# Kernel optimization log

Measured on AMD Instinct MI355X. Metric: run time of the kernel, lower is better.

## Reference

```python
import jax, jax.numpy as jnp
import numpy as np

S_DIM, A_DIM, H_DIM = 256, 18, 256
E, NS, B = 5, 10, 4096  # ensemble, MC samples, batch


def setup_inputs() -> dict:
    key = jax.random.key(0)
    ks = iter(jax.random.split(key, 40))
    def kaiming(k, shape):
        return jax.random.normal(k, shape, jnp.float32) * np.float32(np.sqrt(2.0 / shape[-1]))
    inp = {
        "state": jax.random.normal(next(ks), (B, S_DIM), jnp.float32),
        "num_samples": NS,
    }
    dims = [(H_DIM, S_DIM), (H_DIM, H_DIM), (A_DIM, H_DIM)]
    for i, (o, ii) in enumerate(dims):
        inp[f"w_mu{i}"] = kaiming(next(ks), (E, o, ii))
        inp[f"w_rho{i}"] = jnp.full((E, o, ii), -3.0, jnp.float32)
        inp[f"b_mu{i}"] = jnp.zeros((E, o), jnp.float32)
        inp[f"b_rho{i}"] = jnp.full((E, o), -3.0, jnp.float32)
        inp[f"w_eps{i}"] = jax.random.normal(next(ks), (E, NS, o, ii), jnp.float32)
        inp[f"b_eps{i}"] = jax.random.normal(next(ks), (E, NS, o), jnp.float32)
    # uncertainty head: Linear(2A->H), ReLU, Linear(H->A), Softplus
    inp["uh_w1"] = kaiming(next(ks), (H_DIM, 2 * A_DIM))
    inp["uh_b1"] = jnp.zeros((H_DIM,), jnp.float32)
    inp["uh_w2"] = kaiming(next(ks), (A_DIM, H_DIM))
    inp["uh_b2"] = jnp.zeros((A_DIM,), jnp.float32)
    # risk head: Linear(3A->H), ReLU, Linear(H->1)
    inp["rh_w1"] = kaiming(next(ks), (H_DIM, 3 * A_DIM))
    inp["rh_b1"] = jnp.zeros((H_DIM,), jnp.float32)
    inp["rh_w2"] = kaiming(next(ks), (1, H_DIM))
    inp["rh_b2"] = jnp.zeros((1,), jnp.float32)
    return inp


def _kl(mu, sigma):
    # KL(N(mu, sigma) || N(0, 1)) summed over param dims -> per-ensemble [E]
    kl = -jnp.log(sigma) + (sigma ** 2 + mu ** 2) * 0.5 - 0.5
    return jnp.sum(kl, axis=tuple(range(1, mu.ndim)))


def _bayes(x, wmu, wrho, bmu, brho, weps, beps):
    # x: [E,S,B,in]; wmu: [E,out,in]; weps: [E,S,out,in]
    wsig = jax.nn.softplus(wrho)
    bsig = jax.nn.softplus(brho)
    w = wmu[:, None] + wsig[:, None] * weps        # [E,S,out,in]
    b = bmu[:, None] + bsig[:, None] * beps        # [E,S,out]
    y = jnp.einsum('esbi,esoi->esbo', x, w) + b[:, :, None, :]
    kl = _kl(wmu, wsig) + _kl(bmu, bsig)           # [E] (same for all MC samples)
    return y, kl


def reference(state, num_samples,
              w_mu0, w_rho0, b_mu0, b_rho0, w_eps0, b_eps0,
              w_mu1, w_rho1, b_mu1, b_rho1, w_eps1, b_eps1,
              w_mu2, w_rho2, b_mu2, b_rho2, w_eps2, b_eps2,
              uh_w1, uh_b1, uh_w2, uh_b2,
              rh_w1, rh_b1, rh_w2, rh_b2):
    e, ns = w_eps0.shape[0], w_eps0.shape[1]
    x = jnp.broadcast_to(state, (e, ns) + state.shape)          # [E,S,B,in]
    x, kl0 = _bayes(x, w_mu0, w_rho0, b_mu0, b_rho0, w_eps0, b_eps0)
    x = jax.nn.relu(x)  # dropout = identity (eval)
    x, kl1 = _bayes(x, w_mu1, w_rho1, b_mu1, b_rho1, w_eps1, b_eps1)
    x = jax.nn.relu(x)
    x, kl2 = _bayes(x, w_mu2, w_rho2, b_mu2, b_rho2, w_eps2, b_eps2)
    net_out = x.mean(axis=1)                                     # [E,B,A]
    q_mean = net_out.mean(axis=0)                                # [B,A]
    q_var = jnp.var(net_out, axis=0, ddof=1)                     # unbiased, as torch .var
    epistemic = q_var
    u_in = jnp.concatenate([q_mean, q_var], axis=-1)             # [B,2A]
    h = jax.nn.relu(u_in @ uh_w1.T + uh_b1)
    aleatoric = jax.nn.softplus(h @ uh_w2.T + uh_b2)             # [B,A]
    total_unc = epistemic + aleatoric
    r_in = jnp.concatenate([q_mean, epistemic, aleatoric], axis=-1)  # [B,3A]
    risk = jax.nn.relu(r_in @ rh_w1.T + rh_b1) @ rh_w2.T + rh_b2     # [B,1]
    s = 2.0 * jnp.sqrt(total_unc)
    lcb, ucb = q_mean - s, q_mean + s
    # total_kl = sum_e ns*kl_e ; divided by (E*num_samples) -> mean over ensemble
    kl_div = jnp.sum(kl0 + kl1 + kl2) / e
    return (q_mean, epistemic, aleatoric, total_unc, lcb, ucb, risk, kl_div)
```

## Files before the change

kernel.cpp:

```cpp
#include <hip/hip_runtime.h>
#include <hip/hip_bf16.h>


typedef __bf16 bf16x8 __attribute__((ext_vector_type(8)));
typedef float f32x4 __attribute__((ext_vector_type(4)));
typedef float f32x16 __attribute__((ext_vector_type(16)));
typedef unsigned short u16x4 __attribute__((ext_vector_type(4)));
typedef unsigned short u16x8 __attribute__((ext_vector_type(8)));

__device__ __forceinline__ unsigned short f2bf(float f) {
  unsigned int u = __builtin_bit_cast(unsigned int, f);
  u += 0x7fffu + ((u >> 16) & 1u);
  return (unsigned short)(u >> 16);
}

__device__ __forceinline__ float softplus_f(float x) {
  return (x > 20.f) ? x : __logf(1.f + __expf(x));
}

__device__ __forceinline__ float klterm(float m, float sg) {
  return -__logf(sg) + (sg * sg + m * m) * 0.5f - 0.5f;
}

__device__ __forceinline__ f32x16 mfma32(bf16x8 a, bf16x8 b, f32x16 c) {
  return __builtin_amdgcn_mfma_f32_32x32x16_bf16(a, b, c, 0, 0, 0);
}

template <int O>
__device__ __forceinline__ float wpanel_body(
    int p, int t, const float* __restrict__ wmu, const float* __restrict__ wrho,
    const float* __restrict__ weps, char* __restrict__ wf,
    char* __restrict__ lb) {
  int es = (O == 256) ? (p >> 3) : p;
  int osub = (O == 256) ? (p & 7) : 0;
  int e = es / 10, s = es - e * 10;
  float kl = 0.f;
  int i = (4 * t) & 255;
  int kt2 = i >> 4, byo = (i & 7) * 2, hi32 = 32 * ((i >> 3) & 1);
#pragma unroll
  for (int j = 0; j < 8; ++j) {
    int o = j * 4 + (t >> 6);
    int og = osub * 32 + o;
    float v[4];
    if (O == 256 || og < O) {
      size_t base = ((size_t)(e * O + og)) * 256 + i;
      f32x4 m4 = *(const f32x4*)(wmu + base);
      f32x4 r4 = *(const f32x4*)(wrho + base);
      f32x4 e4 = *(const f32x4*)(weps + ((size_t)((e * 10 + s) * O + og)) * 256 + i);
#pragma unroll
      for (int c = 0; c < 4; ++c) {
        float m = m4[c];
        float sg = softplus_f(r4[c]);
        v[c] = m + sg * e4[c];
        if (s == 0) kl += klterm(m, sg);
      }
    } else {
#pragma unroll
      for (int c = 0; c < 4; ++c) v[c] = 0.f;
    }
    u16x4 pk = {f2bf(v[0]), f2bf(v[1]), f2bf(v[2]), f2bf(v[3])};
    *(u16x4*)(lb + kt2 * 1024 + (o + hi32) * 16 + byo) = pk;
  }
  __syncthreads();
  char* dst = wf + (size_t)p * 16384;
#pragma unroll
  for (int j = 0; j < 4; ++j) {
    int idx = j * 256 + t;
    *(u16x8*)(dst + idx * 16) = *(const u16x8*)(lb + idx * 16);
  }
  return kl;
}

__device__ __forceinline__ void scvt_body(int gid, const float* __restrict__ s,
                                          unsigned short* __restrict__ d) {
  const f32x4* p = (const f32x4*)(s + (size_t)gid * 8);
  f32x4 x0 = p[0], x1 = p[1];
  u16x8 v = {f2bf(x0.x), f2bf(x0.y), f2bf(x0.z), f2bf(x0.w),
             f2bf(x1.x), f2bf(x1.y), f2bf(x1.z), f2bf(x1.w)};
  *(u16x8*)(d + (size_t)gid * 8) = v;
}

__global__ __launch_bounds__(256) void prep_kernel(
    const float* __restrict__ state, unsigned short* __restrict__ stateb,
    const float* __restrict__ wmu0, const float* __restrict__ wrho0,
    const float* __restrict__ weps0, char* __restrict__ W0f,
    const float* __restrict__ wmu1, const float* __restrict__ wrho1,
    const float* __restrict__ weps1, char* __restrict__ W1f,
    const float* __restrict__ wmu2, const float* __restrict__ wrho2,
    const float* __restrict__ weps2, char* __restrict__ W2f,
    const float* __restrict__ bmu0, const float* __restrict__ brho0,
    const float* __restrict__ beps0, const float* __restrict__ bmu1,
    const float* __restrict__ brho1, const float* __restrict__ beps1,
    const float* __restrict__ bmu2, const float* __restrict__ brho2,
    const float* __restrict__ beps2, float* __restrict__ bias0,
    float* __restrict__ bias1, float* __restrict__ bias2,
    float* __restrict__ partials) {
  __shared__ char lb[16384];
  int bid = blockIdx.x, t = threadIdx.x;
  float kl = 0.f;
  if (bid < 512) {
    scvt_body(bid * 256 + t, state, stateb);
  } else if (bid < 912) {
    kl = wpanel_body<256>(bid - 512, t, wmu0, wrho0, weps0, W0f, lb);
  } else if (bid < 1312) {
    kl = wpanel_body<256>(bid - 912, t, wmu1, wrho1, weps1, W1f, lb);
  } else if (bid < 1362) {
    kl = wpanel_body<18>(bid - 1312, t, wmu2, wrho2, weps2, W2f, lb);
  } else {
    int gid = (bid - 1362) * 256 + t;
    if (gid < 12800) {
      int es = gid >> 8, o = gid & 255, e = es / 10, s = es - e * 10;
      float m = bmu0[e * 256 + o];
      float sg = softplus_f(brho0[e * 256 + o]);
      bias0[gid] = m + sg * beps0[(e * 10 + s) * 256 + o];
      if (s == 0) kl = klterm(m, sg);
    } else if (gid < 25600) {
      int id = gid - 12800;
      int es = id >> 8, o = id & 255, e = es / 10, s = es - e * 10;
      float m = bmu1[e * 256 + o];
      float sg = softplus_f(brho1[e * 256 + o]);
      bias1[id] = m + sg * beps1[(e * 10 + s) * 256 + o];
      if (s == 0) kl = klterm(m, sg);
    } else if (gid < 27200) {
      int id = gid - 25600;
      int es = id >> 5, o = id & 31, e = es / 10, s = es - e * 10;
      if (o < 18) {
        float m = bmu2[e * 18 + o];
        float sg = softplus_f(brho2[e * 18 + o]);
        bias2[id] = m + sg * beps2[(e * 10 + s) * 18 + o];
        if (s == 0) kl = klterm(m, sg);
      } else {
        bias2[id] = 0.f;
      }
    }
  }
#pragma unroll
  for (int m = 32; m >= 1; m >>= 1) kl += __shfl_xor(kl, m);
  __shared__ float wsum[4];
  if ((t & 63) == 0) wsum[t >> 6] = kl;
  __syncthreads();
  if (t == 0) partials[bid] = wsum[0] + wsum[1] + wsum[2] + wsum[3];
}

__device__ __forceinline__ void mlp_layer1o(const char* __restrict__ wA,
                                            const float* __restrict__ bias_es,
                                            int w, char* __restrict__ buf,
                                            int lane) {
  const char* ap = wA + (size_t)w * 16384;
  int lo = lane * 16;
  f32x16 acc0, acc1, acc2, acc3;
#pragma unroll
  for (int c = 0; c < 16; ++c) {
    acc0[c] = 0.f; acc1[c] = 0.f; acc2[c] = 0.f; acc3[c] = 0.f;
  }

  bf16x8 ac = *(const bf16x8*)(ap + lo);
  bf16x8 b0c = *(const bf16x8*)(buf + lo);
  bf16x8 b1c = *(const bf16x8*)(buf + 16384 + lo);
  bf16x8 b2c = *(const bf16x8*)(buf + 32768 + lo);
  bf16x8 b3c = *(const bf16x8*)(buf + 49152 + lo);
#pragma unroll
  for (int kp = 0; kp < 8; ++kp) {
    bf16x8 an = *(const bf16x8*)(ap + (2 * kp + 1) * 1024 + lo);
    bf16x8 b0n = *(const bf16x8*)(buf + (2 * kp + 1) * 1024 + lo);
    bf16x8 b1n = *(const bf16x8*)(buf + 16384 + (2 * kp + 1) * 1024 + lo);
    bf16x8 b2n = *(const bf16x8*)(buf + 32768 + (2 * kp + 1) * 1024 + lo);
    bf16x8 b3n = *(const bf16x8*)(buf + 49152 + (2 * kp + 1) * 1024 + lo);
    __builtin_amdgcn_s_setprio(1);
    acc0 = mfma32(ac, b0c, acc0);
    acc1 = mfma32(ac, b1c, acc1);
    acc2 = mfma32(ac, b2c, acc2);
    acc3 = mfma32(ac, b3c, acc3);
    __builtin_amdgcn_s_setprio(0);
    if (kp < 7) {
      ac = *(const bf16x8*)(ap + (2 * kp + 2) * 1024 + lo);
      b0c = *(const bf16x8*)(buf + (2 * kp + 2) * 1024 + lo);
      b1c = *(const bf16x8*)(buf + 16384 + (2 * kp + 2) * 1024 + lo);
      b2c = *(const bf16x8*)(buf + 32768 + (2 * kp + 2) * 1024 + lo);
      b3c = *(const bf16x8*)(buf + 49152 + (2 * kp + 2) * 1024 + lo);
    }
    __builtin_amdgcn_s_setprio(1);
    acc0 = mfma32(an, b0n, acc0);
    acc1 = mfma32(an, b1n, acc1);
    acc2 = mfma32(an, b2n, acc2);
    acc3 = mfma32(an, b3n, acc3);
    __builtin_amdgcn_s_setprio(0);
  }
  __syncthreads();

  int hi = lane >> 5, bcol = lane & 31;
  int obt = w * 32;
  auto epi = [&](const f32x16& A, int bt) {
    char* fb = buf + (size_t)(bt * 16) * 1024;
#pragma unroll
    for (int q = 0; q < 4; ++q) {
      int o0 = obt + 8 * q + 4 * hi;
      f32x4 bv = *(const f32x4*)(bias_es + o0);
      float v0 = fmaxf(A[4 * q + 0] + bv.x, 0.f);
      float v1 = fmaxf(A[4 * q + 1] + bv.y, 0.f);
      float v2 = fmaxf(A[4 * q + 2] + bv.z, 0.f);
      float v3 = fmaxf(A[4 * q + 3] + bv.w, 0.f);
      u16x4 pk = {f2bf(v0), f2bf(v1), f2bf(v2), f2bf(v3)};
      int kt2t = o0 >> 4;
      *(u16x4*)(fb + kt2t * 1024 + (bcol + 32 * (q & 1)) * 16 + 8 * hi) = pk;
    }
  };
  epi(acc0, 0);
  epi(acc1, 1);
  epi(acc2, 2);
  epi(acc3, 3);
  __syncthreads();
}

__global__ __launch_bounds__(512, 4) void mlp_fused(
    const unsigned short* __restrict__ stateb, const char* __restrict__ W0f,
    const char* __restrict__ W1f, const char* __restrict__ W2f,
    const float* __restrict__ bias0, const float* __restrict__ bias1,
    const float* __restrict__ bias2, float* __restrict__ y2) {
  __shared__ char buf[65536];
  int tid = threadIdx.x, w = tid >> 6, lane = tid & 63;
  int lo = lane * 16;

  int bid = blockIdx.x;
  int lin = (bid & 7) * 200 + (bid >> 3);
  int es = lin >> 5, b0 = (lin & 31) * 128;

#pragma unroll
  for (int it = 0; it < 8; ++it) {
    int F = it * 8 + w, bt = F >> 4, kt2 = F & 15;
    const unsigned short* src =
        stateb + (size_t)(b0 + bt * 32 + (lane & 31)) * 256 + kt2 * 16 + (lane >> 5) * 8;
    *(u16x8*)(buf + F * 1024 + lo) = *(const u16x8*)src;
  }
  __syncthreads();

  mlp_layer1o(W0f + (size_t)es * 131072, bias0 + es * 256, w, buf, lane);
  mlp_layer1o(W1f + (size_t)es * 131072, bias1 + es * 256, w, buf, lane);

  if (w < 4) {
    int bt2 = w;
    f32x16 acc2;
#pragma unroll
    for (int c = 0; c < 16; ++c) acc2[c] = 0.f;
    const char* b2k = buf + (size_t)bt2 * 16384;
    const char* w2p = W2f + (size_t)es * 16384;
#pragma unroll
    for (int k = 0; k < 16; ++k) {
      bf16x8 a = *(const bf16x8*)(w2p + k * 1024 + lo);
      bf16x8 bb = *(const bf16x8*)(b2k + k * 1024 + lo);
      acc2 = mfma32(a, bb, acc2);
    }
    int hi = lane >> 5, bcol = lane & 31;
    int b_idx = b0 + bt2 * 32 + bcol;
    float* yp = y2 + ((size_t)es * 4096 + b_idx) * 20;
    float s[16];
#pragma unroll
    for (int q = 0; q < 4; ++q) {
      f32x4 bv = *(const f32x4*)(bias2 + es * 32 + 8 * q + 4 * hi);
      s[4 * q + 0] = acc2[4 * q + 0] + bv.x;
      s[4 * q + 1] = acc2[4 * q + 1] + bv.y;
      s[4 * q + 2] = acc2[4 * q + 2] + bv.z;
      s[4 * q + 3] = acc2[4 * q + 3] + bv.w;
    }
    if (hi == 0) {
      f32x4 v0 = {s[0], s[1], s[2], s[3]};
      f32x4 v1 = {s[4], s[5], s[6], s[7]};
      float2 v2 = {s[8], s[9]};
      *(f32x4*)(yp) = v0;
      *(f32x4*)(yp + 8) = v1;
      *(float2*)(yp + 16) = v2;
    } else {
      f32x4 v0 = {s[0], s[1], s[2], s[3]};
      f32x4 v1 = {s[4], s[5], s[6], s[7]};
      *(f32x4*)(yp + 4) = v0;
      *(f32x4*)(yp + 12) = v1;
    }
  }
}

__global__ __launch_bounds__(256) void heads_kernel(
    const float* __restrict__ y2, const float* __restrict__ partials,
    const float* __restrict__ uh_w1, const float* __restrict__ uh_b1,
    const float* __restrict__ uh_w2, const float* __restrict__ uh_b2,
    const float* __restrict__ rh_w1, const float* __restrict__ rh_b1,
    const float* __restrict__ rh_w2, const float* __restrict__ rh_b2,
    float* __restrict__ out) {
  int bid = blockIdx.x, t = threadIdx.x;
  if (bid == 512) {
    if (t < 64) {
      float acc = 0.f;
      for (int i = t; i < 1469; i += 64) acc += partials[i];
#pragma unroll
      for (int m = 32; m >= 1; m >>= 1) acc += __shfl_xor(acc, m);
      if (t == 0) out[446464] = acc * 0.2f;
    }
    return;
  }
  int b0 = bid * 8;

  __shared__ float ysh[8][1004];
  __shared__ float qsE[8][90];
  __shared__ float rin[8][56];
  __shared__ float h[8][260];

  for (int i = t; i < 2000; i += 256) {
    int r = i / 250, c = i - r * 250;
    int es_t = c / 5, part = c - es_t * 5;
    *(f32x4*)(&ysh[r][c * 4]) =
        *(const f32x4*)(y2 + ((size_t)es_t * 4096 + b0 + r) * 20 + part * 4);
  }
  __syncthreads();

  for (int i = t; i < 720; i += 256) {
    int r = i / 90, ae = i - r * 90;
    int a = ae / 5, e = ae - a * 5;
    float v = 0.f;
#pragma unroll
    for (int s = 0; s < 10; ++s) v += ysh[r][(e * 10 + s) * 20 + a];
    qsE[r][ae] = v * 0.1f;
  }
  __syncthreads();

  if (t < 144) {
    int r = t / 18, a = t - (t / 18) * 18;
    float qs = 0.f, qq = 0.f;
#pragma unroll
    for (int e = 0; e < 5; ++e) {
      float v = qsE[r][a * 5 + e];
      qs += v;
      qq += v * v;
    }
    float mean = qs * 0.2f;
    float var = fmaxf((qq - 5.f * mean * mean) * 0.25f, 0.f);
    rin[r][a] = mean;
    rin[r][18 + a] = var;
    out[(b0 + r) * 18 + a] = mean;
    out[73728 + (b0 + r) * 18 + a] = var;
  }
  __syncthreads();

  {
    f32x4 wv[9];
    const f32x4* wr = (const f32x4*)(uh_w1 + t * 36);
#pragma unroll
    for (int j = 0; j < 9; ++j) wv[j] = wr[j];
    float bb = uh_b1[t];
#pragma unroll
    for (int r = 0; r < 8; ++r) {
      float acc = bb;
#pragma unroll
      for (int j = 0; j < 9; ++j) {
        acc += wv[j].x * rin[r][j * 4] + wv[j].y * rin[r][j * 4 + 1] +
               wv[j].z * rin[r][j * 4 + 2] + wv[j].w * rin[r][j * 4 + 3];
      }
      h[r][t] = fmaxf(acc, 0.f);
    }
  }
  __syncthreads();

  if (t < 144) {
    int r = t / 18, a = t - (t / 18) * 18;
    float p = 0.f;
    const f32x4* w2r = (const f32x4*)(uh_w2 + a * 256);
#pragma unroll
    for (int j = 0; j < 64; ++j) {
      f32x4 wv = w2r[j];
      f32x4 hv = *(const f32x4*)(&h[r][j * 4]);
      p += wv.x * hv.x + wv.y * hv.y + wv.z * hv.z + wv.w * hv.w;
    }
    float alea = softplus_f(p + uh_b2[a]);
    float qm = rin[r][a], epi = rin[r][18 + a];
    float tu = epi + alea;
    float s2 = 2.f * sqrtf(tu);
    int b = b0 + r;
    out[2 * 73728 + b * 18 + a] = alea;
    out[3 * 73728 + b * 18 + a] = tu;
    out[4 * 73728 + b * 18 + a] = qm - s2;
    out[5 * 73728 + b * 18 + a] = qm + s2;
    rin[r][36 + a] = alea;
  }
  __syncthreads();

  {
    float w1v[54];
    const float2* wr2 = (const float2*)(rh_w1 + t * 54);
#pragma unroll
    for (int j = 0; j < 27; ++j) {
      float2 wv = wr2[j];
      w1v[j * 2] = wv.x;
      w1v[j * 2 + 1] = wv.y;
    }
    float bb = rh_b1[t];
#pragma unroll
    for (int r = 0; r < 8; ++r) {
      float acc = bb;
#pragma unroll
      for (int j = 0; j < 54; ++j) acc += w1v[j] * rin[r][j];
      h[r][t] = fmaxf(acc, 0.f);
    }
  }
  __syncthreads();

  if (t < 8) {
    float p = 0.f;
    const f32x4* w2r = (const f32x4*)(rh_w2);
#pragma unroll
    for (int j = 0; j < 64; ++j) {
      f32x4 wv = w2r[j];
      f32x4 hv = *(const f32x4*)(&h[t][j * 4]);
      p += wv.x * hv.x + wv.y * hv.y + wv.z * hv.z + wv.w * hv.w;
    }
    out[6 * 73728 + b0 + t] = p + rh_b2[0];
  }
}

extern "C" void kernel_launch(void* const* d_in, const int* in_sizes, int n_in,
                              void* d_out, int out_size, void* d_ws, size_t ws_size,
                              hipStream_t stream) {
  const float* state = (const float*)d_in[0];
  const float* w_mu0 = (const float*)d_in[2];
  const float* w_rho0 = (const float*)d_in[3];
  const float* b_mu0 = (const float*)d_in[4];
  const float* b_rho0 = (const float*)d_in[5];
  const float* w_eps0 = (const float*)d_in[6];
  const float* b_eps0 = (const float*)d_in[7];
  const float* w_mu1 = (const float*)d_in[8];
  const float* w_rho1 = (const float*)d_in[9];
  const float* b_mu1 = (const float*)d_in[10];
  const float* b_rho1 = (const float*)d_in[11];
  const float* w_eps1 = (const float*)d_in[12];
  const float* b_eps1 = (const float*)d_in[13];
  const float* w_mu2 = (const float*)d_in[14];
  const float* w_rho2 = (const float*)d_in[15];
  const float* b_mu2 = (const float*)d_in[16];
  const float* b_rho2 = (const float*)d_in[17];
  const float* w_eps2 = (const float*)d_in[18];
  const float* b_eps2 = (const float*)d_in[19];
  const float* uh_w1 = (const float*)d_in[20];
  const float* uh_b1 = (const float*)d_in[21];
  const float* uh_w2 = (const float*)d_in[22];
  const float* uh_b2 = (const float*)d_in[23];
  const float* rh_w1 = (const float*)d_in[24];
  const float* rh_b1 = (const float*)d_in[25];
  const float* rh_w2 = (const float*)d_in[26];
  const float* rh_b2 = (const float*)d_in[27];
  float* out = (float*)d_out;

  char* ws = (char*)d_ws;
  unsigned short* stateb = (unsigned short*)ws;
  char* W0f = ws + 2097152;
  char* W1f = W0f + 6553600;
  char* W2f = W1f + 6553600;
  float* bias0 = (float*)(W2f + 819200);
  float* bias1 = bias0 + 12800;
  float* bias2 = bias1 + 12800;
  float* y2 = bias2 + 1600;
  float* klpart = y2 + (size_t)50 * 4096 * 20;

  prep_kernel<<<1469, 256, 0, stream>>>(
      state, stateb, w_mu0, w_rho0, w_eps0, W0f, w_mu1, w_rho1, w_eps1, W1f,
      w_mu2, w_rho2, w_eps2, W2f, b_mu0, b_rho0, b_eps0, b_mu1, b_rho1, b_eps1,
      b_mu2, b_rho2, b_eps2, bias0, bias1, bias2, klpart);
  mlp_fused<<<1600, 512, 0, stream>>>(stateb, W0f, W1f, W2f, bias0, bias1,
                                      bias2, y2);
  heads_kernel<<<513, 256, 0, stream>>>(y2, klpart, uh_w1, uh_b1, uh_w2, uh_b2,
                                        rh_w1, rh_b1, rh_w2, rh_b2, out);
}
```

Measured before the change: 108.9 us.

## Stage weight tiles into LDS with async global_load_lds pipeline, halve batch tile

Packed layer-0/1 weights are reordered by k-slice so each 8 KB k-step across all output tiles is contiguous. The fused MLP kernel now streams these slices into a 4-deep LDS ring with global_load_lds, overlapping loads with MFMA instead of reading weights straight from global memory. The batch tile per block drops from 128 to 64 and the grid doubles to 3200 blocks, which halves the activation LDS footprint. The cost is a barrier per k-step, hand-written waitcnt bookkeeping, and twice as many weight reads from L2 across blocks.

```diff
diff --git a/kernel.cpp b/kernel.cpp
--- a/kernel.cpp
+++ b/kernel.cpp
@@ -24,6 +24,12 @@
 
 __device__ __forceinline__ f32x16 mfma32(bf16x8 a, bf16x8 b, f32x16 c) {
   return __builtin_amdgcn_mfma_f32_32x32x16_bf16(a, b, c, 0, 0, 0);
+}
+
+__device__ __forceinline__ void stage1k(char* l, const char* g) {
+  __builtin_amdgcn_global_load_lds(
+      (const __attribute__((address_space(1))) unsigned int*)g,
+      (__attribute__((address_space(3))) unsigned int*)l, 16, 0, 0);
 }
 
 template <int O>
@@ -62,11 +68,21 @@
     *(u16x4*)(lb + kt2 * 1024 + (o + hi32) * 16 + byo) = pk;
   }
   __syncthreads();
-  char* dst = wf + (size_t)p * 16384;
-#pragma unroll
-  for (int j = 0; j < 4; ++j) {
-    int idx = j * 256 + t;
-    *(u16x8*)(dst + idx * 16) = *(const u16x8*)(lb + idx * 16);
+  if (O == 256) {
+    char* base = wf + (size_t)es * 131072 + (size_t)osub * 1024;
+#pragma unroll
+    for (int j = 0; j < 4; ++j) {
+      int idx = j * 256 + t;
+      int k2 = idx >> 6, u = idx & 63;
+      *(u16x8*)(base + k2 * 8192 + u * 16) = *(const u16x8*)(lb + idx * 16);
+    }
+  } else {
+    char* dst = wf + (size_t)p * 16384;
+#pragma unroll
+    for (int j = 0; j < 4; ++j) {
+      int idx = j * 256 + t;
+      *(u16x8*)(dst + idx * 16) = *(const u16x8*)(lb + idx * 16);
+    }
   }
   return kl;
 }
@@ -142,107 +158,107 @@
   if (t == 0) partials[bid] = wsum[0] + wsum[1] + wsum[2] + wsum[3];
 }
 
-__device__ __forceinline__ void mlp_layer1o(const char* __restrict__ wA,
-                                            const float* __restrict__ bias_es,
-                                            int w, char* __restrict__ buf,
-                                            int lane) {
-  const char* ap = wA + (size_t)w * 16384;
-  int lo = lane * 16;
-  f32x16 acc0, acc1, acc2, acc3;
-#pragma unroll
-  for (int c = 0; c < 16; ++c) {
-    acc0[c] = 0.f; acc1[c] = 0.f; acc2[c] = 0.f; acc3[c] = 0.f;
-  }
-
-  bf16x8 ac = *(const bf16x8*)(ap + lo);
-  bf16x8 b0c = *(const bf16x8*)(buf + lo);
-  bf16x8 b1c = *(const bf16x8*)(buf + 16384 + lo);
-  bf16x8 b2c = *(const bf16x8*)(buf + 32768 + lo);
-  bf16x8 b3c = *(const bf16x8*)(buf + 49152 + lo);
-#pragma unroll
-  for (int kp = 0; kp < 8; ++kp) {
-    bf16x8 an = *(const bf16x8*)(ap + (2 * kp + 1) * 1024 + lo);
-    bf16x8 b0n = *(const bf16x8*)(buf + (2 * kp + 1) * 1024 + lo);
-    bf16x8 b1n = *(const bf16x8*)(buf + 16384 + (2 * kp + 1) * 1024 + lo);
-    bf16x8 b2n = *(const bf16x8*)(buf + 32768 + (2 * kp + 1) * 1024 + lo);
-    bf16x8 b3n = *(const bf16x8*)(buf + 49152 + (2 * kp + 1) * 1024 + lo);
-    __builtin_amdgcn_s_setprio(1);
-    acc0 = mfma32(ac, b0c, acc0);
-    acc1 = mfma32(ac, b1c, acc1);
-    acc2 = mfma32(ac, b2c, acc2);
-    acc3 = mfma32(ac, b3c, acc3);
-    __builtin_amdgcn_s_setprio(0);
-    if (kp < 7) {
-      ac = *(const bf16x8*)(ap + (2 * kp + 2) * 1024 + lo);
-      b0c = *(const bf16x8*)(buf + (2 * kp + 2) * 1024 + lo);
-      b1c = *(const bf16x8*)(buf + 16384 + (2 * kp + 2) * 1024 + lo);
-      b2c = *(const bf16x8*)(buf + 32768 + (2 * kp + 2) * 1024 + lo);
-      b3c = *(const bf16x8*)(buf + 49152 + (2 * kp + 2) * 1024 + lo);
-    }
-    __builtin_amdgcn_s_setprio(1);
-    acc0 = mfma32(an, b0n, acc0);
-    acc1 = mfma32(an, b1n, acc1);
-    acc2 = mfma32(an, b2n, acc2);
-    acc3 = mfma32(an, b3n, acc3);
-    __builtin_amdgcn_s_setprio(0);
-  }
-  __syncthreads();
-
-  int hi = lane >> 5, bcol = lane & 31;
-  int obt = w * 32;
-  auto epi = [&](const f32x16& A, int bt) {
-    char* fb = buf + (size_t)(bt * 16) * 1024;
-#pragma unroll
-    for (int q = 0; q < 4; ++q) {
-      int o0 = obt + 8 * q + 4 * hi;
-      f32x4 bv = *(const f32x4*)(bias_es + o0);
-      float v0 = fmaxf(A[4 * q + 0] + bv.x, 0.f);
-      float v1 = fmaxf(A[4 * q + 1] + bv.y, 0.f);
-      float v2 = fmaxf(A[4 * q + 2] + bv.z, 0.f);
-      float v3 = fmaxf(A[4 * q + 3] + bv.w, 0.f);
-      u16x4 pk = {f2bf(v0), f2bf(v1), f2bf(v2), f2bf(v3)};
-      int kt2t = o0 >> 4;
-      *(u16x4*)(fb + kt2t * 1024 + (bcol + 32 * (q & 1)) * 16 + 8 * hi) = pk;
-    }
-  };
-  epi(acc0, 0);
-  epi(acc1, 1);
-  epi(acc2, 2);
-  epi(acc3, 3);
-  __syncthreads();
-}
-
 __global__ __launch_bounds__(512, 4) void mlp_fused(
     const unsigned short* __restrict__ stateb, const char* __restrict__ W0f,
     const char* __restrict__ W1f, const char* __restrict__ W2f,
     const float* __restrict__ bias0, const float* __restrict__ bias1,
     const float* __restrict__ bias2, float* __restrict__ y2) {
-  __shared__ char buf[65536];
+  __shared__ char lds[65536];
+  char* bact = lds;
+  char* aslt = lds + 32768;
   int tid = threadIdx.x, w = tid >> 6, lane = tid & 63;
   int lo = lane * 16;
 
   int bid = blockIdx.x;
-  int lin = (bid & 7) * 200 + (bid >> 3);
-  int es = lin >> 5, b0 = (lin & 31) * 128;
-
-#pragma unroll
-  for (int it = 0; it < 8; ++it) {
+  int lin = (bid & 7) * 400 + (bid >> 3);
+  int es = lin >> 6, b0 = (lin & 63) * 64;
+
+  const char* w0src = W0f + (size_t)es * 131072;
+  const char* w1src = W1f + (size_t)es * 131072;
+
+  stage1k(aslt + w * 1024, w0src + w * 1024 + lo);
+  stage1k(aslt + 8192 + w * 1024, w0src + 8192 + w * 1024 + lo);
+  stage1k(aslt + 16384 + w * 1024, w0src + 16384 + w * 1024 + lo);
+
+#pragma unroll
+  for (int it = 0; it < 4; ++it) {
     int F = it * 8 + w, bt = F >> 4, kt2 = F & 15;
     const unsigned short* src =
         stateb + (size_t)(b0 + bt * 32 + (lane & 31)) * 256 + kt2 * 16 + (lane >> 5) * 8;
-    *(u16x8*)(buf + F * 1024 + lo) = *(const u16x8*)src;
-  }
-  __syncthreads();
-
-  mlp_layer1o(W0f + (size_t)es * 131072, bias0 + es * 256, w, buf, lane);
-  mlp_layer1o(W1f + (size_t)es * 131072, bias1 + es * 256, w, buf, lane);
-
-  if (w < 4) {
+    *(u16x8*)(bact + F * 1024 + lo) = *(const u16x8*)src;
+  }
+  asm volatile("s_waitcnt lgkmcnt(0)" ::: "memory");
+  __builtin_amdgcn_s_barrier();
+
+  auto body = [&](int g, const char* ssrc, f32x16& c0, f32x16& c1) {
+    __builtin_amdgcn_s_barrier();
+    if (ssrc)
+      stage1k(aslt + ((g + 3) & 3) * 8192 + w * 1024,
+              ssrc + (size_t)((g + 3) & 15) * 8192 + w * 1024 + lo);
+    bf16x8 a = *(const bf16x8*)(aslt + (g & 3) * 8192 + w * 1024 + lo);
+    bf16x8 bv0 = *(const bf16x8*)(bact + (g & 15) * 1024 + lo);
+    bf16x8 bv1 = *(const bf16x8*)(bact + 16384 + (g & 15) * 1024 + lo);
+    __builtin_amdgcn_s_setprio(1);
+    c0 = mfma32(a, bv0, c0);
+    c1 = mfma32(a, bv1, c1);
+    __builtin_amdgcn_s_setprio(0);
+  };
+
+  auto epi_layer = [&](const float* bias_es, const f32x16& A0, const f32x16& A1) {
+    __builtin_amdgcn_s_barrier();
+    int hi = lane >> 5, bcol = lane & 31;
+    int obt = w * 32;
+    auto epi1 = [&](const f32x16& A, int bt) {
+      char* fb = bact + (size_t)(bt * 16) * 1024;
+#pragma unroll
+      for (int q = 0; q < 4; ++q) {
+        int o0 = obt + 8 * q + 4 * hi;
+        f32x4 bv = *(const f32x4*)(bias_es + o0);
+        float v0 = fmaxf(A[4 * q + 0] + bv.x, 0.f);
+        float v1 = fmaxf(A[4 * q + 1] + bv.y, 0.f);
+        float v2 = fmaxf(A[4 * q + 2] + bv.z, 0.f);
+        float v3 = fmaxf(A[4 * q + 3] + bv.w, 0.f);
+        u16x4 pk = {f2bf(v0), f2bf(v1), f2bf(v2), f2bf(v3)};
+        int kt2t = o0 >> 4;
+        *(u16x4*)(fb + kt2t * 1024 + (bcol + 32 * (q & 1)) * 16 + 8 * hi) = pk;
+      }
+    };
+    epi1(A0, 0);
+    epi1(A1, 1);
+    asm volatile("s_waitcnt lgkmcnt(0)" ::: "memory");
+    __builtin_amdgcn_s_barrier();
+  };
+
+  f32x16 p0, p1;
+#pragma unroll
+  for (int c = 0; c < 16; ++c) { p0[c] = 0.f; p1[c] = 0.f; }
+#pragma unroll
+  for (int g = 0; g < 16; ++g) {
+    asm volatile("s_waitcnt vmcnt(2)" ::: "memory");
+    body(g, (g + 3 < 16) ? w0src : w1src, p0, p1);
+  }
+  epi_layer(bias0 + es * 256, p0, p1);
+
+  f32x16 q0, q1;
+#pragma unroll
+  for (int c = 0; c < 16; ++c) { q0[c] = 0.f; q1[c] = 0.f; }
+#pragma unroll
+  for (int g = 16; g < 30; ++g) {
+    asm volatile("s_waitcnt vmcnt(2)" ::: "memory");
+    body(g, (g + 3 < 32) ? w1src : nullptr, q0, q1);
+  }
+  asm volatile("s_waitcnt vmcnt(1)" ::: "memory");
+  body(30, nullptr, q0, q1);
+  asm volatile("s_waitcnt vmcnt(0)" ::: "memory");
+  body(31, nullptr, q0, q1);
+  epi_layer(bias1 + es * 256, q0, q1);
+
+  if (w < 2) {
     int bt2 = w;
     f32x16 acc2;
 #pragma unroll
     for (int c = 0; c < 16; ++c) acc2[c] = 0.f;
-    const char* b2k = buf + (size_t)bt2 * 16384;
+    const char* b2k = bact + (size_t)bt2 * 16384;
     const char* w2p = W2f + (size_t)es * 16384;
 #pragma unroll
     for (int k = 0; k < 16; ++k) {
@@ -461,7 +477,7 @@
       state, stateb, w_mu0, w_rho0, w_eps0, W0f, w_mu1, w_rho1, w_eps1, W1f,
       w_mu2, w_rho2, w_eps2, W2f, b_mu0, b_rho0, b_eps0, b_mu1, b_rho1, b_eps1,
       b_mu2, b_rho2, b_eps2, bias0, bias1, bias2, klpart);
-  mlp_fused<<<1600, 512, 0, stream>>>(stateb, W0f, W1f, W2f, bias0, bias1,
+  mlp_fused<<<3200, 512, 0, stream>>>(stateb, W0f, W1f, W2f, bias0, bias1,
                                       bias2, y2);
   heads_kernel<<<513, 256, 0, stream>>>(y2, klpart, uh_w1, uh_b1, uh_w2, uh_b2,
                                         rh_w1, rh_b1, rh_w2, rh_b2, out);
```

Result: slower. 121.6 us (+11.6%).
